# Optimization experiments

Measured on AMD Instinct MI355X. Metric: run time of the kernel, lower is better.

Reference implementation:

```python
import jax, jax.numpy as jnp
import numpy as np

DIM = 256
HEADS = 8
DIM_HEAD = 64
EPS = 1e-12  # F.normalize eps


def rms_norm(x, w, dim):
    # F.normalize over channel dim (axis=1) * weight * sqrt(dim)
    n = jnp.sqrt(jnp.sum(x * x, axis=1, keepdims=True))
    xn = x / jnp.maximum(n, EPS)
    return xn * w[None, :, None, None] * (dim ** 0.5)


def setup_inputs() -> dict:
    key = jax.random.key(0)
    ks = jax.random.split(key, 4)
    hd = HEADS * DIM_HEAD
    return {
        "x": jax.random.normal(ks[0], (16, DIM, 64, 64), dtype=jnp.float32),
        "norm_w": jnp.ones((DIM,), jnp.float32),
        "qkv_w": jax.random.normal(ks[1], (3 * hd, DIM), jnp.float32) * (DIM ** -0.5),
        "out_w": jax.random.normal(ks[2], (DIM, hd), jnp.float32) * (hd ** -0.5),
        "out_b": jnp.zeros((DIM,), jnp.float32),
        "out_norm_w": jnp.ones((DIM,), jnp.float32),
    }


def reference(x, norm_w, qkv_w, out_w, out_b, out_norm_w):
    b, c, H, W = x.shape
    n = H * W
    scale = DIM_HEAD ** -0.5

    xn = rms_norm(x, norm_w, DIM)
    # 1x1 conv == channel matmul: [3hd, c] x [b, c, H, W]
    qkv = jnp.einsum('oc,bchw->bohw', qkv_w, xn)
    q, k, v = jnp.split(qkv, 3, axis=1)

    def to_heads(t):
        # b (h d) x y -> b h d n
        return t.reshape(b, HEADS, DIM_HEAD, n)

    q = jax.nn.softmax(to_heads(q), axis=2) * scale  # softmax over feature dim d
    k = jax.nn.softmax(to_heads(k), axis=3)          # softmax over spatial n
    v = to_heads(v)

    ctx = jnp.einsum('bhdn,bhen->bhde', k, v)   # [b,h,d,e]
    out = jnp.einsum('bhde,bhdn->bhen', ctx, q) # [b,h,e,n]
    out = out.reshape(b, HEADS * DIM_HEAD, H, W)

    out = jnp.einsum('oc,bchw->bohw', out_w, out) + out_b[None, :, None, None]
    return rms_norm(out, out_norm_w, DIM)
```

## Files before the change

kernel.cpp:

```cpp
#include <hip/hip_runtime.h>

#define C_ 256
#define N_ 4096
#define NH_ 8

typedef unsigned short u16;
typedef unsigned int u32;
typedef __attribute__((ext_vector_type(8))) short s8v;
typedef __attribute__((ext_vector_type(4))) float f4v;

#define MFMA16 __builtin_amdgcn_mfma_f32_16x16x32_bf16

__device__ __forceinline__ float bf2f(u16 b){ union{u32 u; float f;} v; v.u=((u32)b)<<16; return v.f; }
__device__ __forceinline__ u16 f2bf(float f){ union{float f; u32 u;} v; v.f=f; return (u16)((v.u + 0x7FFFu + ((v.u>>16)&1u))>>16); }

__device__ __forceinline__ void gl_lds16(const u16* g, u16* l){
  __builtin_amdgcn_global_load_lds((const __attribute__((address_space(1))) u32*)g,
                                   (__attribute__((address_space(3))) u32*)l, 16, 0, 0);
}

__global__ __launch_bounds__(256) void k_prep(const float* __restrict__ x, const float* __restrict__ nw,
                                              u16* __restrict__ xnT){
  __shared__ float red[256];
  __shared__ float nws[256];
  const int tid = threadIdx.x;
  nws[tid] = nw[tid];
  const int blk = blockIdx.x, b = blk>>6, n0 = (blk&63)*64;
  const int cq = tid>>6, px = tid&63;
  const float* xp = x + (size_t)b*(C_*N_) + (size_t)(cq*64)*N_ + n0 + px;
  float v[64]; float s = 0.f;
  #pragma unroll
  for (int i=0;i<64;i++){ float t = xp[(size_t)i*N_]; v[i]=t; s = fmaf(t,t,s); }
  red[tid] = s;
  __syncthreads();
  const float st = red[px] + red[64+px] + red[128+px] + red[192+px];
  const float r = 16.0f / fmaxf(sqrtf(st), 1e-12f);
  u16* o = xnT + ((size_t)b*4096 + n0 + px)*256 + cq*64;
  #pragma unroll
  for (int i=0;i<64;i+=2){
    *(u32*)(o+i) = (u32)f2bf(v[i]*r*nws[cq*64+i]) | ((u32)f2bf(v[i+1]*r*nws[cq*64+i+1])<<16);
  }
}

__global__ __launch_bounds__(256) void k_wconv(const float* __restrict__ qkvw, const float* __restrict__ ow,
                                               u16* __restrict__ wqkv, u16* __restrict__ owb){
  int q = blockIdx.x*256 + threadIdx.x;
  int i = q*4;
  const float4 f4 = (i < 393216) ? *(const float4*)&qkvw[i] : *(const float4*)&ow[i-393216];
  u32 lo = (u32)f2bf(f4.x) | ((u32)f2bf(f4.y)<<16);
  u32 hi = (u32)f2bf(f4.z) | ((u32)f2bf(f4.w)<<16);
  u16* dst = (i < 393216) ? (wqkv + i) : (owb + (i-393216));
  *(u32*)dst = lo;
  *(u32*)(dst+2) = hi;
}

__global__ __launch_bounds__(256,3) void k_kv(const u16* __restrict__ xnT, const u16* __restrict__ wqkv,
    u16* __restrict__ ctxp, float* __restrict__ Mp, float* __restrict__ Sp){
  __shared__ u16 xs[64*256];
  __shared__ u16 pbuf[64*72];
  __shared__ u16 vbuf[64*72];
  const int idx = blockIdx.x;
  const int ch = idx&7, h = (idx>>3)&7, b = idx>>6;
  const int tid=threadIdx.x, w=tid>>6, l=tid&63, l15=l&15, lg=l>>4;
  const int swl = (l15&7)<<4;
  const u16* xb  = xnT + (size_t)b*(4096*256);
  const int srow = (l>>5);
  const int scolB = (l&31)*16;
  s8v ak[8], av[8];
  {
    const u16* wkp = wqkv + (size_t)(512 + h*64 + w*16 + l15)*256 + lg*8;
    #pragma unroll
    for (int cs=0; cs<8; cs++){ ak[cs] = *(const s8v*)(wkp + cs*32); av[cs] = *(const s8v*)(wkp + 131072 + cs*32); }
  }
  int colOff[8];
  #pragma unroll
  for (int cs=0; cs<8; cs++) colOff[cs] = (((cs<<6)+(lg<<4)) ^ swl)>>1;

  f4v acc[4];
  #pragma unroll
  for (int et=0;et<4;et++) acc[et] = (f4v){0.f,0.f,0.f,0.f};
  float ps[4] = {0.f,0.f,0.f,0.f};

  {
    const int n0 = ch*512;
    #pragma unroll
    for (int i=0;i<8;i++){
      int rloc = w*16 + i*2 + srow;
      int scol = scolB ^ ((rloc&7)<<4);
      gl_lds16(xb + (size_t)(n0+rloc)*256 + (scol>>1), &xs[(w*16+i*2)*256]);
    }
  }

  for (int t=0; t<8; ++t){
    __syncthreads();
    f4v kacc[4], vacc[4];
    #pragma unroll
    for (int ns=0;ns<4;ns++){ kacc[ns]=(f4v){0.f,0.f,0.f,0.f}; vacc[ns]=(f4v){0.f,0.f,0.f,0.f}; }
    #pragma unroll
    for (int cs=0; cs<8; cs++){
      #pragma unroll
      for (int ns=0; ns<4; ns++){
        s8v bfr = *(const s8v*)&xs[(ns*16+l15)*256 + colOff[cs]];
        kacc[ns] = MFMA16(ak[cs], bfr, kacc[ns], 0,0,0);
        vacc[ns] = MFMA16(av[cs], bfr, vacc[ns], 0,0,0);
      }
    }
    #pragma unroll
    for (int j=0;j<4;j++){
      const int row = w*16 + lg*4 + j;
      #pragma unroll
      for (int ns=0;ns<4;ns++){
        float e = __expf(kacc[ns][j] - 30.0f);
        ps[j] += e;
        pbuf[row*72 + ns*16+l15] = f2bf(e);
        vbuf[row*72 + ns*16+l15] = f2bf(vacc[ns][j]);
      }
    }
    __syncthreads();
    if (t<7){
      const int n0 = ch*512 + (t+1)*64;
      #pragma unroll
      for (int i=0;i<8;i++){
        int rloc = w*16 + i*2 + srow;
        int scol = scolB ^ ((rloc&7)<<4);
        gl_lds16(xb + (size_t)(n0+rloc)*256 + (scol>>1), &xs[(w*16+i*2)*256]);
      }
    }
    #pragma unroll
    for (int ks=0; ks<2; ks++){
      s8v af = *(const s8v*)(pbuf + (w*16+l15)*72 + ks*32 + lg*8);
      #pragma unroll
      for (int et=0; et<4; et++){
        s8v bv = *(const s8v*)(vbuf + (et*16+l15)*72 + ks*32 + lg*8);
        acc[et] = MFMA16(af, bv, acc[et], 0,0,0);
      }
    }
  }
  u16* cp = ctxp + (((size_t)ch*16 + b)*8 + h)*4096;
  #pragma unroll
  for (int et=0; et<4; et++)
    #pragma unroll
    for (int j=0;j<4;j++)
      cp[(w*16+lg*4+j)*64 + et*16+l15] = f2bf(acc[et][j]);
  #pragma unroll
  for (int j=0;j<4;j++){
    float s = ps[j];
    s += __shfl_xor(s,1); s += __shfl_xor(s,2);
    s += __shfl_xor(s,4); s += __shfl_xor(s,8);
    ps[j] = s;
  }
  if (l15==0){
    #pragma unroll
    for (int j=0;j<4;j++){
      int rg = (b*8+h)*64 + w*16 + lg*4 + j;
      Mp[ch*8192+rg]=30.0f; Sp[ch*8192+rg]=ps[j];
    }
  }
}

__global__ __launch_bounds__(256) void k_comb(const u16* __restrict__ ctxp, const float* __restrict__ Mp,
    const float* __restrict__ Sp, u16* __restrict__ ctxD){
  __shared__ float fs[8][64];
  __shared__ float iSs[64];
  const int bh = blockIdx.x, tid = threadIdx.x;
  if (tid < 64){
    float m[8];
    float Mg = -1e30f;
    #pragma unroll
    for (int ch=0;ch<8;ch++){ m[ch] = Mp[ch*8192 + bh*64 + tid]; Mg = fmaxf(Mg, m[ch]); }
    float Sg = 0.f;
    #pragma unroll
    for (int ch=0;ch<8;ch++){
      float fv = __expf(m[ch]-Mg);
      fs[ch][tid] = fv;
      Sg += Sp[ch*8192 + bh*64 + tid]*fv;
    }
    iSs[tid] = 1.0f / Sg;
  }
  __syncthreads();
  const int d = tid>>2, e0 = (tid&3)*16;
  u16* op = ctxD + (size_t)bh*4096 + d*64 + e0;
  const float fsc = iSs[d];
  #pragma unroll
  for (int i=0;i<16;i++){
    float v = 0.f;
    #pragma unroll
    for (int ch=0;ch<8;ch++)
      v += bf2f(ctxp[(size_t)ch*524288 + (size_t)bh*4096 + d*64 + e0+i]) * fs[ch][d];
    op[i] = f2bf(v * fsc);
  }
}

__global__ __launch_bounds__(256) void k_g(const u16* __restrict__ owb, const u16* __restrict__ ctxD,
                                           u16* __restrict__ G){
  const int bh = blockIdx.x, h = bh&7;
  const int tid = threadIdx.x, w = tid>>6, l = tid&63, l15 = l&15, lg = l>>4;
  s8v a[4][2], bD[4][2];
  #pragma unroll
  for (int mt=0; mt<4; mt++)
    #pragma unroll
    for (int ks=0; ks<2; ks++)
      a[mt][ks] = *(const s8v*)(owb + (size_t)(w*64+mt*16+l15)*512 + h*64 + ks*32 + lg*8);
  #pragma unroll
  for (int dt=0; dt<4; dt++)
    #pragma unroll
    for (int ks=0; ks<2; ks++)
      bD[dt][ks] = *(const s8v*)(ctxD + (size_t)bh*4096 + (dt*16+l15)*64 + ks*32 + lg*8);
  f4v acc[4][4];
  #pragma unroll
  for (int mt=0;mt<4;mt++)
    #pragma unroll
    for (int dt=0;dt<4;dt++) acc[mt][dt] = (f4v){0.f,0.f,0.f,0.f};
  #pragma unroll
  for (int ks=0; ks<2; ks++)
    #pragma unroll
    for (int mt=0; mt<4; mt++)
      #pragma unroll
      for (int dt=0; dt<4; dt++)
        acc[mt][dt] = MFMA16(a[mt][ks], bD[dt][ks], acc[mt][dt], 0,0,0);
  u16* gp = G + (size_t)bh*16384;
  #pragma unroll
  for (int mt=0; mt<4; mt++)
    #pragma unroll
    for (int dt=0; dt<4; dt++)
      #pragma unroll
      for (int j=0; j<4; j++)
        gp[(w*64 + mt*16 + lg*4 + j)*64 + dt*16 + l15] = f2bf(acc[mt][dt][j]);
}

__global__ __launch_bounds__(512,2) void k_qout(const u16* __restrict__ xnT, const u16* __restrict__ wqkv,
    const u16* __restrict__ Gg, const float* __restrict__ ob, const float* __restrict__ onw,
    float* __restrict__ out){
  __shared__ u16 WQb[2][64*256];
  __shared__ u16 Gb[2][256*64];
  __shared__ u16 qa[8][1024];
  const int tid = threadIdx.x;
  const int w=tid>>6, l=tid&63, l15=l&15, lg=l>>4;
  const int blk=blockIdx.x, b=blk>>5, n0=(blk&31)*128 + w*16;
  const u16* xb = xnT + ((size_t)b*4096 + n0)*256;
  const u16* Gbase = Gg + (size_t)b*8*16384;
  u16* qaw = qa[w];
  const int wqRow0 = (l>>5);
  const int wqColB = (l&31)*16;
  const int gRow0  = (l>>3);
  const int gColB  = (l&7)*16;
  s8v ax[8];
  #pragma unroll
  for (int cs=0;cs<8;cs++) ax[cs] = *(const s8v*)(xb + (size_t)l15*256 + cs*32 + lg*8);
  f4v oacc[16];
  #pragma unroll
  for (int mt=0;mt<16;mt++) oacc[mt] = (f4v){0.f,0.f,0.f,0.f};

  #pragma unroll
  for (int i=0;i<4;i++){
    int row = (i*8+w)*2 + wqRow0;
    int scol = wqColB ^ ((row&15)<<4);
    gl_lds16(wqkv + (size_t)row*256 + (scol>>1), &WQb[0][(i*8+w)*512]);
  }
  #pragma unroll
  for (int i=0;i<4;i++){
    int row = (i*8+w)*8 + gRow0;
    int scol = gColB ^ ((row&7)<<4);
    gl_lds16(Gbase + (size_t)row*64 + (scol>>1), &Gb[0][(i*8+w)*512]);
  }

  for (int h=0; h<8; ++h){
    const int p = h&1;
    __syncthreads();
    if (h<7){
      const u16* wqg = wqkv + (size_t)(h+1)*64*256;
      const u16* gg  = Gbase + (size_t)(h+1)*16384;
      #pragma unroll
      for (int i=0;i<4;i++){
        int row = (i*8+w)*2 + wqRow0;
        int scol = wqColB ^ ((row&15)<<4);
        gl_lds16(wqg + (size_t)row*256 + (scol>>1), &WQb[p^1][(i*8+w)*512]);
      }
      #pragma unroll
      for (int i=0;i<4;i++){
        int row = (i*8+w)*8 + gRow0;
        int scol = gColB ^ ((row&7)<<4);
        gl_lds16(gg + (size_t)row*64 + (scol>>1), &Gb[p^1][(i*8+w)*512]);
      }
    }
    f4v qacc[4];
    #pragma unroll
    for (int dt=0;dt<4;dt++) qacc[dt] = (f4v){0.f,0.f,0.f,0.f};
    #pragma unroll
    for (int dt=0; dt<4; dt++){
      #pragma unroll
      for (int cs=0; cs<8; cs++){
        s8v bw = *(const s8v*)&WQb[p][(dt*16+l15)*256 + ((((cs<<6)|(lg<<4)) ^ (l15<<4))>>1)];
        qacc[dt] = MFMA16(ax[cs], bw, qacc[dt], 0,0,0);
      }
    }
    #pragma unroll
    for (int j=0;j<4;j++){
      float m = fmaxf(fmaxf(qacc[0][j],qacc[1][j]),fmaxf(qacc[2][j],qacc[3][j]));
      #pragma unroll
      for (int d=1; d<16; d<<=1) m = fmaxf(m, __shfl_xor(m, d));
      float s = 0.f;
      #pragma unroll
      for (int dt=0;dt<4;dt++){ float e=__expf(qacc[dt][j]-m); qacc[dt][j]=e; s+=e; }
      #pragma unroll
      for (int d=1; d<16; d<<=1) s += __shfl_xor(s, d);
      float inv = 0.125f/s;
      #pragma unroll
      for (int dt=0;dt<4;dt++){
        int row = lg*4+j;
        qaw[((row<<6) + dt*16 + l15) ^ ((row&7)<<3)] = f2bf(qacc[dt][j]*inv);
      }
    }
    #pragma unroll
    for (int ks=0; ks<2; ks++){
      s8v ba = *(const s8v*)&qaw[(l15<<6) + ((((ks<<6)|(lg<<4)) ^ ((l15&7)<<4))>>1)];
      #pragma unroll
      for (int mt=0; mt<16; mt++){
        s8v aw = *(const s8v*)&Gb[p][(mt*16+l15)*64 + ((((ks<<6)|(lg<<4)) ^ ((l15&7)<<4))>>1)];
        oacc[mt] = MFMA16(aw, ba, oacc[mt], 0,0,0);
      }
    }
  }
  float ss = 0.f;
  #pragma unroll
  for (int mt=0;mt<16;mt++){
    const float4 o4 = *(const float4*)&ob[mt*16 + lg*4];
    #pragma unroll
    for (int j=0;j<4;j++){
      float v = oacc[mt][j] + ((const float*)&o4)[j];
      oacc[mt][j] = v;
      ss = fmaf(v,v,ss);
    }
  }
  ss += __shfl_xor(ss, 16);
  ss += __shfl_xor(ss, 32);
  const float r = 16.0f / fmaxf(sqrtf(ss), 1e-12f);
  float* op = out + (size_t)b*(256*4096) + n0 + l15;
  #pragma unroll
  for (int mt=0;mt<16;mt++){
    const float4 w4 = *(const float4*)&onw[mt*16 + lg*4];
    #pragma unroll
    for (int j=0;j<4;j++){
      int cout = mt*16+lg*4+j;
      op[(size_t)cout*4096] = oacc[mt][j] * r * ((const float*)&w4)[j];
    }
  }
}

extern "C" void kernel_launch(void* const* d_in, const int* in_sizes, int n_in,
                              void* d_out, int out_size, void* d_ws, size_t ws_size,
                              hipStream_t stream){
  const float* x    = (const float*)d_in[0];
  const float* nw   = (const float*)d_in[1];
  const float* qkvw = (const float*)d_in[2];
  const float* ow   = (const float*)d_in[3];
  const float* ob   = (const float*)d_in[4];
  const float* onw  = (const float*)d_in[5];
  float* out = (float*)d_out;
  char* ws = (char*)d_ws;
  u16*   xnT  = (u16*)(ws);
  u16*   wqkv = (u16*)(ws + 33554432);
  u16*   owb  = (u16*)(ws + 34340864);
  u16*   ctxD = (u16*)(ws + 34603008);
  u16*   ctxp = (u16*)(ws + 35651584);
  u16*   G    = ctxp;
  float* Mp   = (float*)(ws + 44040192);
  float* Sp   = (float*)(ws + 44302336);
  (void)in_sizes; (void)n_in; (void)out_size; (void)ws_size;

  k_wconv<<<512, 256, 0, stream>>>(qkvw, ow, wqkv, owb);
  k_prep <<<1024, 256, 0, stream>>>(x, nw, xnT);
  k_kv   <<<1024, 256, 0, stream>>>(xnT, wqkv, ctxp, Mp, Sp);
  k_comb <<<128, 256, 0, stream>>>(ctxp, Mp, Sp, ctxD);
  k_g    <<<128, 256, 0, stream>>>(owb, ctxD, G);
  k_qout <<<512, 512, 0, stream>>>(xnT, wqkv, G, ob, onw, out);
}
```

Measured before the change: 162.2 us.

## Split q-out work across wave pairs with single-buffered LDS for occupancy

Reworks k_qout so each block covers 64 tokens with pairs of waves. Each wave computes half of the q feature dims and half of the output channels, and the partial softmax sums and squared norms are exchanged through shared memory. The double-buffered weight and G tiles become single buffers, which shrinks LDS use and register pressure so more blocks can be resident, and the grid doubles to 1024 blocks. The softmax drops its per-token max reduction in favour of a fixed shift of 30. That shift is only safe while q values stay in a bounded range, and the change also adds extra barriers and repeats the G loads in every block.

Measured after the change: 169.4 us. 4.4% more time.

```diff
diff --git a/kernel.cpp b/kernel.cpp
--- a/kernel.cpp
+++ b/kernel.cpp
@@ -228,103 +228,112 @@
         gp[(w*64 + mt*16 + lg*4 + j)*64 + dt*16 + l15] = f2bf(acc[mt][dt][j]);
 }
 
-__global__ __launch_bounds__(512,2) void k_qout(const u16* __restrict__ xnT, const u16* __restrict__ wqkv,
+__global__ __launch_bounds__(512,4) void k_qout(const u16* __restrict__ xnT, const u16* __restrict__ wqkv,
     const u16* __restrict__ Gg, const float* __restrict__ ob, const float* __restrict__ onw,
     float* __restrict__ out){
-  __shared__ u16 WQb[2][64*256];
-  __shared__ u16 Gb[2][256*64];
-  __shared__ u16 qa[8][1024];
+  __shared__ u16 WQ[64*256];
+  __shared__ u16 Gs[256*64];
+  __shared__ u16 qa[4][1024];
+  __shared__ float pp[4][2][16];
+  __shared__ float ssb[4][2][16];
   const int tid = threadIdx.x;
   const int w=tid>>6, l=tid&63, l15=l&15, lg=l>>4;
-  const int blk=blockIdx.x, b=blk>>5, n0=(blk&31)*128 + w*16;
+  const int g=w&3, half=w>>2;
+  const int blk=blockIdx.x, b=blk>>6, n0=(blk&63)*64;
   const u16* xb = xnT + ((size_t)b*4096 + n0)*256;
   const u16* Gbase = Gg + (size_t)b*8*16384;
-  u16* qaw = qa[w];
+  u16* qag = qa[g];
   const int wqRow0 = (l>>5);
   const int wqColB = (l&31)*16;
   const int gRow0  = (l>>3);
   const int gColB  = (l&7)*16;
   s8v ax[8];
   #pragma unroll
-  for (int cs=0;cs<8;cs++) ax[cs] = *(const s8v*)(xb + (size_t)l15*256 + cs*32 + lg*8);
-  f4v oacc[16];
-  #pragma unroll
-  for (int mt=0;mt<16;mt++) oacc[mt] = (f4v){0.f,0.f,0.f,0.f};
+  for (int cs=0;cs<8;cs++) ax[cs] = *(const s8v*)(xb + (size_t)(g*16+l15)*256 + cs*32 + lg*8);
+  f4v oacc[8];
+  #pragma unroll
+  for (int mt=0;mt<8;mt++) oacc[mt] = (f4v){0.f,0.f,0.f,0.f};
 
   #pragma unroll
   for (int i=0;i<4;i++){
     int row = (i*8+w)*2 + wqRow0;
     int scol = wqColB ^ ((row&15)<<4);
-    gl_lds16(wqkv + (size_t)row*256 + (scol>>1), &WQb[0][(i*8+w)*512]);
+    gl_lds16(wqkv + (size_t)row*256 + (scol>>1), &WQ[(i*8+w)*512]);
   }
   #pragma unroll
   for (int i=0;i<4;i++){
     int row = (i*8+w)*8 + gRow0;
     int scol = gColB ^ ((row&7)<<4);
-    gl_lds16(Gbase + (size_t)row*64 + (scol>>1), &Gb[0][(i*8+w)*512]);
+    gl_lds16(Gbase + (size_t)row*64 + (scol>>1), &Gs[(i*8+w)*512]);
   }
 
   for (int h=0; h<8; ++h){
-    const int p = h&1;
+    __syncthreads();
+    if (h>0){
+      const u16* gg = Gbase + (size_t)h*16384;
+      #pragma unroll
+      for (int i=0;i<4;i++){
+        int row = (i*8+w)*8 + gRow0;
+        int scol = gColB ^ ((row&7)<<4);
+        gl_lds16(gg + (size_t)row*64 + (scol>>1), &Gs[(i*8+w)*512]);
+      }
+    }
+    f4v qacc[2];
+    qacc[0] = (f4v){0.f,0.f,0.f,0.f};
+    qacc[1] = (f4v){0.f,0.f,0.f,0.f};
+    #pragma unroll
+    for (int dt2=0; dt2<2; dt2++){
+      const int drow = (half*2+dt2)*16 + l15;
+      #pragma unroll
+      for (int cs=0; cs<8; cs++){
+        s8v bw = *(const s8v*)&WQ[drow*256 + ((((cs<<6)|(lg<<4)) ^ (l15<<4))>>1)];
+        qacc[dt2] = MFMA16(ax[cs], bw, qacc[dt2], 0,0,0);
+      }
+    }
+    float sj[4];
+    #pragma unroll
+    for (int j=0;j<4;j++){
+      float e0 = __expf(qacc[0][j]-30.0f);
+      float e1 = __expf(qacc[1][j]-30.0f);
+      qacc[0][j]=e0; qacc[1][j]=e1;
+      float s = e0+e1;
+      s += __shfl_xor(s,1); s += __shfl_xor(s,2);
+      s += __shfl_xor(s,4); s += __shfl_xor(s,8);
+      sj[j] = s;
+      if (l15==0) pp[g][half][lg*4+j] = s;
+    }
+    __syncthreads();
+    #pragma unroll
+    for (int j=0;j<4;j++){
+      const float inv = 0.125f/(sj[j] + pp[g][half^1][lg*4+j]);
+      const int row = lg*4+j;
+      qag[((row<<6) + (half*2+0)*16 + l15) ^ ((row&7)<<3)] = f2bf(qacc[0][j]*inv);
+      qag[((row<<6) + (half*2+1)*16 + l15) ^ ((row&7)<<3)] = f2bf(qacc[1][j]*inv);
+    }
     __syncthreads();
     if (h<7){
       const u16* wqg = wqkv + (size_t)(h+1)*64*256;
-      const u16* gg  = Gbase + (size_t)(h+1)*16384;
       #pragma unroll
       for (int i=0;i<4;i++){
         int row = (i*8+w)*2 + wqRow0;
         int scol = wqColB ^ ((row&15)<<4);
-        gl_lds16(wqg + (size_t)row*256 + (scol>>1), &WQb[p^1][(i*8+w)*512]);
-      }
-      #pragma unroll
-      for (int i=0;i<4;i++){
-        int row = (i*8+w)*8 + gRow0;
-        int scol = gColB ^ ((row&7)<<4);
-        gl_lds16(gg + (size_t)row*64 + (scol>>1), &Gb[p^1][(i*8+w)*512]);
-      }
-    }
-    f4v qacc[4];
-    #pragma unroll
-    for (int dt=0;dt<4;dt++) qacc[dt] = (f4v){0.f,0.f,0.f,0.f};
-    #pragma unroll
-    for (int dt=0; dt<4; dt++){
-      #pragma unroll
-      for (int cs=0; cs<8; cs++){
-        s8v bw = *(const s8v*)&WQb[p][(dt*16+l15)*256 + ((((cs<<6)|(lg<<4)) ^ (l15<<4))>>1)];
-        qacc[dt] = MFMA16(ax[cs], bw, qacc[dt], 0,0,0);
-      }
-    }
-    #pragma unroll
-    for (int j=0;j<4;j++){
-      float m = fmaxf(fmaxf(qacc[0][j],qacc[1][j]),fmaxf(qacc[2][j],qacc[3][j]));
-      #pragma unroll
-      for (int d=1; d<16; d<<=1) m = fmaxf(m, __shfl_xor(m, d));
-      float s = 0.f;
-      #pragma unroll
-      for (int dt=0;dt<4;dt++){ float e=__expf(qacc[dt][j]-m); qacc[dt][j]=e; s+=e; }
-      #pragma unroll
-      for (int d=1; d<16; d<<=1) s += __shfl_xor(s, d);
-      float inv = 0.125f/s;
-      #pragma unroll
-      for (int dt=0;dt<4;dt++){
-        int row = lg*4+j;
-        qaw[((row<<6) + dt*16 + l15) ^ ((row&7)<<3)] = f2bf(qacc[dt][j]*inv);
+        gl_lds16(wqg + (size_t)row*256 + (scol>>1), &WQ[(i*8+w)*512]);
       }
     }
     #pragma unroll
     for (int ks=0; ks<2; ks++){
-      s8v ba = *(const s8v*)&qaw[(l15<<6) + ((((ks<<6)|(lg<<4)) ^ ((l15&7)<<4))>>1)];
-      #pragma unroll
-      for (int mt=0; mt<16; mt++){
-        s8v aw = *(const s8v*)&Gb[p][(mt*16+l15)*64 + ((((ks<<6)|(lg<<4)) ^ ((l15&7)<<4))>>1)];
+      s8v ba = *(const s8v*)&qag[(l15<<6) + ((((ks<<6)|(lg<<4)) ^ ((l15&7)<<4))>>1)];
+      #pragma unroll
+      for (int mt=0; mt<8; mt++){
+        s8v aw = *(const s8v*)&Gs[(half*128 + mt*16 + l15)*64 + ((((ks<<6)|(lg<<4)) ^ ((l15&7)<<4))>>1)];
         oacc[mt] = MFMA16(aw, ba, oacc[mt], 0,0,0);
       }
     }
   }
   float ss = 0.f;
   #pragma unroll
-  for (int mt=0;mt<16;mt++){
-    const float4 o4 = *(const float4*)&ob[mt*16 + lg*4];
+  for (int mt=0;mt<8;mt++){
+    const float4 o4 = *(const float4*)&ob[half*128 + mt*16 + lg*4];
     #pragma unroll
     for (int j=0;j<4;j++){
       float v = oacc[mt][j] + ((const float*)&o4)[j];
@@ -334,14 +343,17 @@
   }
   ss += __shfl_xor(ss, 16);
   ss += __shfl_xor(ss, 32);
-  const float r = 16.0f / fmaxf(sqrtf(ss), 1e-12f);
-  float* op = out + (size_t)b*(256*4096) + n0 + l15;
-  #pragma unroll
-  for (int mt=0;mt<16;mt++){
-    const float4 w4 = *(const float4*)&onw[mt*16 + lg*4];
-    #pragma unroll
-    for (int j=0;j<4;j++){
-      int cout = mt*16+lg*4+j;
+  if (l < 16) ssb[g][half][l15] = ss;
+  __syncthreads();
+  const float sst = ss + ssb[g][half^1][l15];
+  const float r = 16.0f / fmaxf(sqrtf(sst), 1e-12f);
+  float* op = out + (size_t)b*(256*4096) + n0 + g*16 + l15;
+  #pragma unroll
+  for (int mt=0;mt<8;mt++){
+    const float4 w4 = *(const float4*)&onw[half*128 + mt*16 + lg*4];
+    #pragma unroll
+    for (int j=0;j<4;j++){
+      int cout = half*128 + mt*16 + lg*4 + j;
       op[(size_t)cout*4096] = oacc[mt][j] * r * ((const float*)&w4)[j];
     }
   }
@@ -373,5 +385,5 @@
   k_kv   <<<1024, 256, 0, stream>>>(xnT, wqkv, ctxp, Mp, Sp);
   k_comb <<<128, 256, 0, stream>>>(ctxp, Mp, Sp, ctxD);
   k_g    <<<128, 256, 0, stream>>>(owb, ctxD, G);
-  k_qout <<<512, 512, 0, stream>>>(xnT, wqkv, G, ob, onw, out);
-}
+  k_qout <<<1024, 512, 0, stream>>>(xnT, wqkv, G, ob, onw, out);
+}
```
